# Performance work log

Measured on AMD Instinct MI355X. Metric: run time of the kernel, lower is better.

## Reference

```python
import jax, jax.numpy as jnp
import numpy as np

CLASS_INTERVAL = 4.0
CLASS_RANGE = 24.0
EPS = 1e-8


def rotate_half(x):
    # pairs adjacent elements: (x0,x1)->(-x1,x0)
    x = x.reshape(x.shape[:-1] + (x.shape[-1] // 2, 2))
    x1, x2 = x[..., 0], x[..., 1]
    return jnp.stack((-x2, x1), axis=-1).reshape(x.shape[:-2] + (-1,))


def rope_1d(x, pos):
    # x: [B, H, N, hd], pos: [N]
    hd = x.shape[-1]
    freqs = 1.0 / (10000.0 ** (jnp.arange(0, hd, 2)[: hd // 2].astype(jnp.float32) / hd))
    f = pos.astype(jnp.float32)[:, None] * freqs[None, :]   # [N, hd/2]
    f = jnp.repeat(f, 2, axis=-1)                            # [N, hd] interleaved
    cos = jnp.cos(f)[None, None]
    sin = jnp.sin(f)[None, None]
    xf = x.astype(jnp.float32)
    return (xf * cos + rotate_half(xf) * sin).astype(x.dtype)


def normalize_and_scale(col, src_min, src_max, tgt_min, tgt_max):
    return (col - src_min) / (src_max - src_min + EPS) * (tgt_max - tgt_min) + tgt_min


def setup_inputs() -> dict:
    key = jax.random.key(0)
    ks = jax.random.split(key, 9)
    N_t, N_h, N_w = 21, 30, 52
    S = N_h * N_w
    dim, enc_dim, N_a = 1536, 768, 32
    scale = 0.02
    return {
        "x": jax.random.normal(ks[0], (1, N_t * S, dim), jnp.float32),
        "encoder_hidden_states": jax.random.normal(ks[1], (N_t, N_a, enc_dim), jnp.float32),
        "x_ref_attn_map": jax.random.uniform(ks[2], (2, N_t * S), jnp.float32),
        "q_w": jax.random.normal(ks[3], (dim, dim), jnp.float32) * scale,
        "q_b": jax.random.normal(ks[4], (dim,), jnp.float32) * scale,
        "kv_w": jax.random.normal(ks[5], (2 * dim, enc_dim), jnp.float32) * scale,
        "kv_b": jax.random.normal(ks[6], (2 * dim,), jnp.float32) * scale,
        "proj_w": jax.random.normal(ks[7], (dim, dim), jnp.float32) * scale,
        "proj_b": jax.random.normal(ks[8], (dim,), jnp.float32) * scale,
        "N_t": N_t,
        "N_h": N_h,
        "N_w": N_w,
        "human_num": 2,
    }


def reference(x, encoder_hidden_states, x_ref_attn_map, q_w, q_b, kv_w, kv_b,
              proj_w, proj_b, N_t, N_h, N_w, human_num):
    assert human_num == 2
    B_orig = x.shape[0]
    S = N_h * N_w
    dim = x.shape[-1]
    num_heads = 12
    head_dim = dim // num_heads
    B = B_orig * N_t

    xf = x.reshape(B, S, dim)                                  # (B*N_t, S, C)
    q = (xf @ q_w.T + q_b).reshape(B, S, num_heads, head_dim)
    q = jnp.transpose(q, (0, 2, 1, 3))                         # [B, H, S, hd]

    # ---- per-pixel speaker routing -> rotary positions (2-speaker branch) ----
    rope_h1 = (0.0, CLASS_INTERVAL)
    rope_h2 = (CLASS_RANGE - CLASS_INTERVAL, CLASS_RANGE)
    rope_bak = CLASS_RANGE / 2.0
    m = x_ref_attn_map                                          # [2, N_t*S]
    human1 = normalize_and_scale(m[0], m[0].min(), m[0].max(), *rope_h1)
    human2 = normalize_and_scale(m[1], m[1].min(), m[1].max(), *rope_h2)
    back = jnp.full_like(human1, rope_bak)
    normalized_map = jnp.stack([human1, human2, back], axis=1)  # [N, 3]
    max_indices = jnp.argmax(m, axis=0)                         # [N]
    normalized_pos = jnp.take_along_axis(normalized_map, max_indices[:, None], axis=1)[:, 0]

    # RoPE on queries over the full (N_t*S) token axis
    q = q.reshape(B_orig, N_t, num_heads, S, head_dim)
    q = jnp.transpose(q, (0, 2, 1, 3, 4)).reshape(B_orig, num_heads, N_t * S, head_dim)
    q = rope_1d(q, normalized_pos)
    q = q.reshape(B_orig, num_heads, N_t, S, head_dim)
    q = jnp.transpose(q, (0, 2, 1, 3, 4)).reshape(B, num_heads, S, head_dim)

    # ---- KV from encoder states, bucket-centre RoPE on K ----
    N_a = encoder_hidden_states.shape[1]
    kv = encoder_hidden_states @ kv_w.T + kv_b                  # [B, N_a, 2*dim]
    kv = kv.reshape(B, N_a, 2, num_heads, head_dim)
    k = jnp.transpose(kv[:, :, 0], (0, 2, 1, 3))                # [B, H, N_a, hd]
    v = jnp.transpose(kv[:, :, 1], (0, 2, 1, 3))

    per_frame = jnp.where(jnp.arange(N_a) < N_a // 2,
                          (rope_h1[0] + rope_h1[1]) / 2.0,
                          (rope_h2[0] + rope_h2[1]) / 2.0).astype(jnp.float32)
    encoder_pos = jnp.tile(per_frame, N_t)                      # [N_t*N_a]

    k = k.reshape(B_orig, N_t, num_heads, N_a, head_dim)
    k = jnp.transpose(k, (0, 2, 1, 3, 4)).reshape(B_orig, num_heads, N_t * N_a, head_dim)
    k = rope_1d(k, encoder_pos)
    k = k.reshape(B_orig, num_heads, N_t, N_a, head_dim)
    k = jnp.transpose(k, (0, 2, 1, 3, 4)).reshape(B, num_heads, N_a, head_dim)

    # ---- cross-attention (KV length is tiny; Q dominates traffic) ----
    scores = jnp.einsum('bhqd,bhkd->bhqk', q, k) / jnp.sqrt(jnp.float32(head_dim))
    probs = jax.nn.softmax(scores, axis=-1)
    out = jnp.einsum('bhqk,bhkd->bqhd', probs, v)               # [B, S, H, hd]

    out = out.reshape(B, S, dim) @ proj_w.T + proj_b
    return out.reshape(B_orig, N_t * S, dim)
```

## Files before the change

kernel.cpp:

```cpp
#include <hip/hip_runtime.h>
#include <cstdio>
#include <cstdint>

#define TOK   32760
#define DIM   1536
#define ENCD  768
#define NA    32
#define NT    21
#define SS    1560
#define HEADS 12
#define HD    128
#define KVROWS (NT * NA)

using f32x4  = __attribute__((ext_vector_type(4))) float;
using bf16x8 = __attribute__((ext_vector_type(8))) short;

__device__ __forceinline__ ushort bf16hi(float f) {
  unsigned u = __float_as_uint(f);
  return (ushort)((u + 0x7FFFu + ((u >> 16) & 1u)) >> 16);
}
__device__ __forceinline__ float bf16tof(ushort h) {
  return __uint_as_float(((unsigned)h) << 16);
}

__device__ __forceinline__ void gload16(const void* g, void* l) {
  __builtin_amdgcn_global_load_lds((const __attribute__((address_space(1))) void*)g,
                                   (__attribute__((address_space(3))) void*)l,
                                   16, 0, 0);
}

__global__ __launch_bounds__(1024) void minmax_pos_kernel(
    const float* __restrict__ m, float* __restrict__ pos, int N) {
  __shared__ float red[4][16];
  __shared__ float fin[4];
  int tid = threadIdx.x;
  float mn0 = 3.4e38f, mx0 = -3.4e38f, mn1 = 3.4e38f, mx1 = -3.4e38f;
  for (int i = tid; i < N; i += 1024) {
    float a = m[i], b = m[N + i];
    mn0 = fminf(mn0, a); mx0 = fmaxf(mx0, a);
    mn1 = fminf(mn1, b); mx1 = fmaxf(mx1, b);
  }
  #pragma unroll
  for (int o = 32; o >= 1; o >>= 1) {
    mn0 = fminf(mn0, __shfl_xor(mn0, o)); mx0 = fmaxf(mx0, __shfl_xor(mx0, o));
    mn1 = fminf(mn1, __shfl_xor(mn1, o)); mx1 = fmaxf(mx1, __shfl_xor(mx1, o));
  }
  int wid = tid >> 6, ln = tid & 63;
  if (ln == 0) { red[0][wid] = mn0; red[1][wid] = mx0; red[2][wid] = mn1; red[3][wid] = mx1; }
  __syncthreads();
  if (tid == 0) {
    float a = red[0][0], b = red[1][0], c = red[2][0], d = red[3][0];
    for (int i = 1; i < 16; i++) {
      a = fminf(a, red[0][i]); b = fmaxf(b, red[1][i]);
      c = fminf(c, red[2][i]); d = fmaxf(d, red[3][i]);
    }
    fin[0] = a; fin[1] = b; fin[2] = c; fin[3] = d;
  }
  __syncthreads();
  float mn0f = fin[0], sc0 = 4.0f / (fin[1] - fin[0] + 1e-8f);
  float mn1f = fin[2], sc1 = 4.0f / (fin[3] - fin[2] + 1e-8f);
  for (int i = tid; i < N; i += 1024) {
    float a = m[i], b = m[N + i];
    float h1 = (a - mn0f) * sc0;
    float h2 = (b - mn1f) * sc1 + 20.0f;
    pos[i] = (a >= b) ? h1 : h2;
  }
}

__global__ void conv_hilo_kernel(const float* __restrict__ in, ushort* __restrict__ out,
                                 int M, int K) {
  int total4 = M * (K / 4);
  for (int idx = blockIdx.x * blockDim.x + threadIdx.x; idx < total4;
       idx += gridDim.x * blockDim.x) {
    int e = idx * 4;
    int row = e / K;
    int k = e - row * K;
    float4 v = *(const float4*)(in + e);
    float fs[4] = {v.x, v.y, v.z, v.w};
    ushort hs[4], ls[4];
    #pragma unroll
    for (int t = 0; t < 4; t++) {
      hs[t] = bf16hi(fs[t]);
      float hf = bf16tof(hs[t]);
      ls[t] = bf16hi(fs[t] - hf);
    }
    ushort* po = out + (size_t)row * (2 * K) + k;
    *(ushort4*)(po)     = make_ushort4(hs[0], hs[1], hs[2], hs[3]);
    *(ushort4*)(po + K) = make_ushort4(ls[0], ls[1], ls[2], ls[3]);
  }
}

__global__ __launch_bounds__(256, 2) void gemm_bf16s_kernel(
    const ushort* __restrict__ A, const ushort* __restrict__ B,
    const float* __restrict__ bias, float* __restrict__ C,
    int M, int N, int K) {
  __shared__ __align__(16) ushort lAh[128][64];
  __shared__ __align__(16) ushort lAl[128][64];
  __shared__ __align__(16) ushort lBh[128][64];
  __shared__ __align__(16) ushort lBl[128][64];
  const int tid = threadIdx.x;
  const int lane = tid & 63;
  const int w = tid >> 6;
  const int wm = w >> 1, wn = w & 1;
  const int quad = lane >> 4, m16 = lane & 15;
  const int r_off = lane >> 3;
  const int g     = lane & 7;
  const int gg8   = (g ^ r_off) * 8;

  int bx = blockIdx.x, by = blockIdx.y;
  {
    const int nx = gridDim.x, ny = gridDim.y;
    if ((ny & 7) == 0) {
      int flat = by * nx + bx;
      int xcd = flat & 7, s = flat >> 3;
      int panel = s / nx;
      bx = s - panel * nx;
      by = panel * 8 + xcd;
    }
  }
  const int m0 = by * 128, n0 = bx * 128;
  const int lda = 2 * K;

  f32x4 acc[4][4];
  #pragma unroll
  for (int i = 0; i < 4; i++)
    #pragma unroll
    for (int j = 0; j < 4; j++) acc[i][j] = (f32x4){0.f, 0.f, 0.f, 0.f};

  const int nIter = K / 64;
  for (int kt = 0; kt < nIter; kt++) {
    const int kH = kt * 64;
    const int kL = K + kt * 64;
    __syncthreads();
    #pragma unroll
    for (int i = 0; i < 4; i++) {
      const int ss = w * 4 + i;
      int rowA = m0 + ss * 8 + r_off; if (rowA >= M) rowA = M - 1;
      const ushort* ar = A + (size_t)rowA * lda;
      gload16(ar + kH + gg8, (char*)&lAh[0][0] + ss * 1024);
      gload16(ar + kL + gg8, (char*)&lAl[0][0] + ss * 1024);
      int rowB = n0 + ss * 8 + r_off; if (rowB >= N) rowB = N - 1;
      const ushort* br = B + (size_t)rowB * lda;
      gload16(br + kH + gg8, (char*)&lBh[0][0] + ss * 1024);
      gload16(br + kL + gg8, (char*)&lBl[0][0] + ss * 1024);
    }
    __syncthreads();
    #pragma unroll
    for (int kk = 0; kk < 2; kk++) {
      const int slot8 = (((kk * 4 + quad) ^ (m16 & 7)) * 8);
      bf16x8 fah[4], fbh[4], ft[4];
      #pragma unroll
      for (int i = 0; i < 4; i++) {
        fah[i] = *(const bf16x8*)(&lAh[wm * 64 + i * 16 + m16][slot8]);
        fbh[i] = *(const bf16x8*)(&lBh[wn * 64 + i * 16 + m16][slot8]);
      }
      #pragma unroll
      for (int i = 0; i < 4; i++)
        #pragma unroll
        for (int j = 0; j < 4; j++)
          acc[i][j] = __builtin_amdgcn_mfma_f32_16x16x32_bf16(fah[i], fbh[j], acc[i][j], 0, 0, 0);
      #pragma unroll
      for (int i = 0; i < 4; i++)
        ft[i] = *(const bf16x8*)(&lBl[wn * 64 + i * 16 + m16][slot8]);
      #pragma unroll
      for (int i = 0; i < 4; i++)
        #pragma unroll
        for (int j = 0; j < 4; j++)
          acc[i][j] = __builtin_amdgcn_mfma_f32_16x16x32_bf16(fah[i], ft[j], acc[i][j], 0, 0, 0);
      #pragma unroll
      for (int i = 0; i < 4; i++)
        ft[i] = *(const bf16x8*)(&lAl[wm * 64 + i * 16 + m16][slot8]);
      #pragma unroll
      for (int i = 0; i < 4; i++)
        #pragma unroll
        for (int j = 0; j < 4; j++)
          acc[i][j] = __builtin_amdgcn_mfma_f32_16x16x32_bf16(ft[i], fbh[j], acc[i][j], 0, 0, 0);
    }
  }
  #pragma unroll
  for (int j = 0; j < 4; j++) {
    const int col = n0 + wn * 64 + j * 16 + m16;
    const float bv = bias[col];
    #pragma unroll
    for (int i = 0; i < 4; i++) {
      const int rbase = m0 + wm * 64 + i * 16 + quad * 4;
      #pragma unroll
      for (int r = 0; r < 4; r++) {
        const int row = rbase + r;
        if (row < M) C[(size_t)row * N + col] = acc[i][j][r] + bv;
      }
    }
  }
}

__global__ __launch_bounds__(512, 2) void gemm256_bf16s_kernel(
    const ushort* __restrict__ A, const ushort* __restrict__ B,
    const float* __restrict__ bias, float* __restrict__ C,
    int M, int N, int K) {
  __shared__ __align__(16) ushort SA[2][256][64];
  __shared__ __align__(16) ushort SB[2][256][64];
  const int tid  = threadIdx.x;
  const int lane = tid & 63;
  const int w    = tid >> 6;
  const int wm   = w >> 2, wn = w & 3;
  const int quad = lane >> 4, m16 = lane & 15;
  const int rsel = lane >> 3;
  const int q    = (lane & 7) ^ rsel;
  int bx = blockIdx.x, by = blockIdx.y;
  {
    const int nx = gridDim.x, ny = gridDim.y;
    if ((ny & 7) == 0) {
      int flat = by * nx + bx;
      int xcd = flat & 7, s = flat >> 3;
      int panel = s / nx;
      bx = s - panel * nx;
      by = panel * 8 + xcd;
    }
  }
  const int m0 = by * 256, n0 = bx * 256;
  const int ld   = 2 * K;
  const int qoff = (q & 3) * 8 + (q >> 2) * K;
  const int shq  = (quad ^ (m16 & 7)) * 8;

  auto stageA = [&](int st, int r0) {
    int R = m0 + r0 + rsel; if (R >= M) R = M - 1;
    gload16(A + (size_t)R * ld + qoff + st * 32, &SA[st & 1][r0][0]);
  };
  auto stageB = [&](int st, int r0) {
    int R = n0 + r0 + rsel; if (R >= N) R = N - 1;
    gload16(B + (size_t)R * ld + qoff + st * 32, &SB[st & 1][r0][0]);
  };
  auto c1 = [&](int st) {
    int G = 2 * w;
    stageB(st, 32 + (G >> 2) * 64 + (G & 3) * 8); G++;
    stageB(st, 32 + (G >> 2) * 64 + (G & 3) * 8);
  };
  auto c2 = [&](int st) {
    int G = 2 * w;
    stageA(st, (G & 7) * 8 + (G >> 3) * 128); G++;
    stageA(st, (G & 7) * 8 + (G >> 3) * 128);
  };
  auto c3 = [&](int st) {
    int G = 2 * w;
    stageA(st, 64 + (G & 7) * 8 + (G >> 3) * 128); G++;
    stageA(st, 64 + (G & 7) * 8 + (G >> 3) * 128);
  };
  auto c4 = [&](int st) {
    int G = 2 * w;
    stageB(st, (G >> 2) * 64 + (G & 3) * 8); G++;
    stageB(st, (G >> 2) * 64 + (G & 3) * 8);
  };

  f32x4 acc[8][4];
  #pragma unroll
  for (int i = 0; i < 8; i++)
    #pragma unroll
    for (int j = 0; j < 4; j++) acc[i][j] = (f32x4){0.f, 0.f, 0.f, 0.f};

  const int nS = K / 32;
  c1(0); c2(0); c3(0); c4(0);
  c1(1); c2(1);
  asm volatile("s_waitcnt vmcnt(4)" ::: "memory");
  __builtin_amdgcn_s_barrier();
  asm volatile("" ::: "memory");

#define PHASE(MH, NH, PF)                                                     \
  {                                                                           \
    PF;                                                                       \
    bf16x8 ah[4], al[4], bh[2], bl[2];                                        \
    _Pragma("unroll")                                                         \
    for (int i = 0; i < 4; i++) {                                             \
      const ushort* ar = &SA[bb][wm * 128 + (MH) * 64 + i * 16 + m16][0];     \
      ah[i] = *(const bf16x8*)(ar + shq);                                     \
      al[i] = *(const bf16x8*)(ar + (shq ^ 32));                              \
    }                                                                         \
    _Pragma("unroll")                                                         \
    for (int j = 0; j < 2; j++) {                                             \
      const ushort* br = &SB[bb][wn * 64 + (NH) * 32 + j * 16 + m16][0];      \
      bh[j] = *(const bf16x8*)(br + shq);                                     \
      bl[j] = *(const bf16x8*)(br + (shq ^ 32));                              \
    }                                                                         \
    __builtin_amdgcn_s_barrier();                                             \
    asm volatile("" ::: "memory");                                            \
    __builtin_amdgcn_s_setprio(1);                                            \
    _Pragma("unroll")                                                         \
    for (int i = 0; i < 4; i++)                                               \
      _Pragma("unroll")                                                       \
      for (int j = 0; j < 2; j++)                                             \
        acc[(MH) * 4 + i][(NH) * 2 + j] = __builtin_amdgcn_mfma_f32_16x16x32_bf16( \
            ah[i], bh[j], acc[(MH) * 4 + i][(NH) * 2 + j], 0, 0, 0);          \
    _Pragma("unroll")                                                         \
    for (int i = 0; i < 4; i++)                                               \
      _Pragma("unroll")                                                       \
      for (int j = 0; j < 2; j++)                                             \
        acc[(MH) * 4 + i][(NH) * 2 + j] = __builtin_amdgcn_mfma_f32_16x16x32_bf16( \
            ah[i], bl[j], acc[(MH) * 4 + i][(NH) * 2 + j], 0, 0, 0);          \
    _Pragma("unroll")                                                         \
    for (int i = 0; i < 4; i++)                                               \
      _Pragma("unroll")                                                       \
      for (int j = 0; j < 2; j++)                                             \
        acc[(MH) * 4 + i][(NH) * 2 + j] = __builtin_amdgcn_mfma_f32_16x16x32_bf16( \
            al[i], bh[j], acc[(MH) * 4 + i][(NH) * 2 + j], 0, 0, 0);          \
    __builtin_amdgcn_s_setprio(0);                                            \
  }

  for (int s = 0; s < nS; s++) {
    const int bb = s & 1;
    PHASE(0, 1, if (s + 1 < nS) c3(s + 1));
    asm volatile("s_waitcnt lgkmcnt(0)" ::: "memory");
    __builtin_amdgcn_s_barrier();
    asm volatile("" ::: "memory");
    PHASE(1, 1, if (s + 1 < nS) c4(s + 1));
    asm volatile("s_waitcnt lgkmcnt(0)" ::: "memory");
    __builtin_amdgcn_s_barrier();
    asm volatile("" ::: "memory");
    PHASE(0, 0, if (s + 2 < nS) c1(s + 2));
    asm volatile("s_waitcnt lgkmcnt(0)" ::: "memory");
    __builtin_amdgcn_s_barrier();
    asm volatile("" ::: "memory");
    PHASE(1, 0, if (s + 2 < nS) c2(s + 2));
    asm volatile("s_waitcnt lgkmcnt(0)" ::: "memory");
    if (s + 2 < nS) { asm volatile("s_waitcnt vmcnt(4)" ::: "memory"); }
    else            { asm volatile("s_waitcnt vmcnt(0)" ::: "memory"); }
    __builtin_amdgcn_s_barrier();
    asm volatile("" ::: "memory");
  }
#undef PHASE

  #pragma unroll
  for (int J = 0; J < 4; J++) {
    const int col = n0 + wn * 64 + J * 16 + m16;
    const float bv = bias[col];
    #pragma unroll
    for (int I = 0; I < 8; I++) {
      const int rbase = m0 + wm * 128 + I * 16 + quad * 4;
      #pragma unroll
      for (int r = 0; r < 4; r++) {
        const int row = rbase + r;
        if (row < M) C[(size_t)row * N + col] = acc[I][J][r] + bv;
      }
    }
  }
}

__global__ __launch_bounds__(64) void attn_kernel(
    const float* __restrict__ q, const float* __restrict__ kv,
    const float* __restrict__ pos, ushort* __restrict__ attA) {
  const int chunk = blockIdx.x;
  const int head  = blockIdx.y;
  const int t     = blockIdx.z;
  const int lane  = threadIdx.x;
  const int a = lane & 31, h = lane >> 5;
  const float L2_10000_64 = 13.287712379549449f / 64.0f;

  float kreg[64];
  const float* krow = kv + (size_t)(t * NA + a) * (2 * DIM) + head * HD + h * 64;
  #pragma unroll
  for (int j = 0; j < 16; j++) ((float4*)kreg)[j] = ((const float4*)krow)[j];
  const float pk = (a < 16) ? 2.0f : 22.0f;
  #pragma unroll
  for (int j = 0; j < 32; j++) {
    int ip = h * 32 + j;
    float fr = exp2f(-(float)ip * L2_10000_64);
    float sn, cs; sincosf(pk * fr, &sn, &cs);
    float x0 = kreg[2 * j], x1 = kreg[2 * j + 1];
    kreg[2 * j]     = x0 * cs - x1 * sn;
    kreg[2 * j + 1] = x1 * cs + x0 * sn;
  }
  float vr0[32], vr1[32];
  const float* vbase = kv + (size_t)(t * NA) * (2 * DIM) + DIM + head * HD;
  #pragma unroll
  for (int aa = 0; aa < 32; aa++) {
    vr0[aa] = vbase[(size_t)aa * (2 * DIM) + lane];
    vr1[aa] = vbase[(size_t)aa * (2 * DIM) + 64 + lane];
  }

  __shared__ float qs[128];
  __shared__ float Ps[32];
  const float myfreq = exp2f(-(float)lane * L2_10000_64);

  for (int r = 0; r < 30; r++) {
    const int n = t * SS + chunk * 30 + r;
    float2 qp = ((const float2*)(q + (size_t)n * DIM + head * HD))[lane];
    float p = pos[n];
    float sn, cs; sincosf(p * myfreq, &sn, &cs);
    qs[2 * lane]     = qp.x * cs - qp.y * sn;
    qs[2 * lane + 1] = qp.y * cs + qp.x * sn;
    __syncthreads();
    float accd = 0.f;
    #pragma unroll
    for (int j4 = 0; j4 < 16; j4++) {
      float4 qq = ((const float4*)(qs + h * 64))[j4];
      accd += qq.x * kreg[j4 * 4] + qq.y * kreg[j4 * 4 + 1] +
              qq.z * kreg[j4 * 4 + 2] + qq.w * kreg[j4 * 4 + 3];
    }
    accd += __shfl_xor(accd, 32);
    accd *= 0.08838834764831845f;
    float mx = accd;
    #pragma unroll
    for (int o = 16; o >= 1; o >>= 1) mx = fmaxf(mx, __shfl_xor(mx, o));
    float e = __expf(accd - mx);
    float sum = e;
    #pragma unroll
    for (int o = 16; o >= 1; o >>= 1) sum += __shfl_xor(sum, o);
    float P = e / sum;
    if (lane < 32) Ps[lane] = P;
    __syncthreads();
    float o0 = 0.f, o1 = 0.f;
    #pragma unroll
    for (int aa = 0; aa < 32; aa++) {
      float pa = Ps[aa];
      o0 += pa * vr0[aa];
      o1 += pa * vr1[aa];
    }
    size_t base = (size_t)n * (2 * DIM);
    int c0 = head * HD + lane;
    ushort h0 = bf16hi(o0); ushort l0 = bf16hi(o0 - bf16tof(h0));
    ushort h1 = bf16hi(o1); ushort l1 = bf16hi(o1 - bf16tof(h1));
    attA[base + c0]            = h0;
    attA[base + DIM + c0]      = l0;
    attA[base + c0 + 64]       = h1;
    attA[base + DIM + c0 + 64] = l1;
    __syncthreads();
  }
}

extern "C" void kernel_launch(void* const* d_in, const int* in_sizes, int n_in,
                              void* d_out, int out_size, void* d_ws, size_t ws_size,
                              hipStream_t stream) {
  const float* x      = (const float*)d_in[0];
  const float* enc    = (const float*)d_in[1];
  const float* xmap   = (const float*)d_in[2];
  const float* q_w    = (const float*)d_in[3];
  const float* q_b    = (const float*)d_in[4];
  const float* kv_w   = (const float*)d_in[5];
  const float* kv_b   = (const float*)d_in[6];
  const float* proj_w = (const float*)d_in[7];
  const float* proj_b = (const float*)d_in[8];
  float* out = (float*)d_out;
  char* ws = (char*)d_ws;

  const size_t OFF_POS  = 0;
  const size_t OFF_APR  = 131072;
  const size_t OFF_Q    = OFF_APR + 201277440;
  const size_t OFF_KV   = OFF_Q   + 201277440;
  const size_t OFF_BQ   = OFF_KV  + 8257536;
  const size_t OFF_BKV  = OFF_BQ  + 9437184;
  const size_t OFF_BP   = OFF_BKV + 9437184;
  const size_t OFF_AKV  = OFF_BP  + 9437184;
  const size_t TOTAL    = OFF_AKV + 2064384;
  if (ws_size < TOTAL) {
    fprintf(stderr, "kernel_launch: ws_size %zu < needed %zu\n", ws_size, TOTAL);
    return;
  }
  float*  pos   = (float*)(ws + OFF_POS);
  ushort* Apr   = (ushort*)(ws + OFF_APR);
  float*  qbuf  = (float*)(ws + OFF_Q);
  float*  kvbuf = (float*)(ws + OFF_KV);
  ushort* Bq    = (ushort*)(ws + OFF_BQ);
  ushort* Bkv   = (ushort*)(ws + OFF_BKV);
  ushort* Bp    = (ushort*)(ws + OFF_BP);
  ushort* Akv   = (ushort*)(ws + OFF_AKV);

  minmax_pos_kernel<<<1, 1024, 0, stream>>>(xmap, pos, TOK);
  conv_hilo_kernel<<<2048, 256, 0, stream>>>(x,      Apr, TOK,    DIM);
  conv_hilo_kernel<<<256,  256, 0, stream>>>(q_w,    Bq,  DIM,    DIM);
  conv_hilo_kernel<<<256,  256, 0, stream>>>(kv_w,   Bkv, 2*DIM,  ENCD);
  conv_hilo_kernel<<<64,   256, 0, stream>>>(enc,    Akv, KVROWS, ENCD);
  conv_hilo_kernel<<<256,  256, 0, stream>>>(proj_w, Bp,  DIM,    DIM);
  gemm256_bf16s_kernel<<<dim3(DIM/256, (TOK+255)/256), 512, 0, stream>>>(
      Apr, Bq, q_b, qbuf, TOK, DIM, DIM);
  gemm_bf16s_kernel<<<dim3(2*DIM/128, (KVROWS+127)/128), 256, 0, stream>>>(
      Akv, Bkv, kv_b, kvbuf, KVROWS, 2*DIM, ENCD);
  attn_kernel<<<dim3(52, HEADS, NT), 64, 0, stream>>>(qbuf, kvbuf, pos, Apr);
  gemm256_bf16s_kernel<<<dim3(DIM/256, (TOK+255)/256), 512, 0, stream>>>(
      Apr, Bp, proj_b, out, TOK, DIM, DIM);
}
```

Baseline: 1.917 ms.

## Replace four-phase interleaved GEMM pipeline with single-phase double-buffered loop

Replaces the 4-phase per-K-step schedule, which interleaved partial global prefetches with quarter-tile MFMA blocks and barriers, with one phase per step. Each step loads all A/B fragments from LDS, runs the full 8x4 MFMA block, then issues the whole prefetch for step s+2 behind a single barrier. This cuts barriers per K-step from four to one or two and simplifies the waitcnt logic. In exchange it loses the fine-grained overlap of global loads with compute and raises fragment register pressure (8+8+4+4 bf16x8 live at once), which could lower occupancy or cause spills.

Result: faster. 1.699 ms (-11.3%).

```diff
diff --git a/kernel.cpp b/kernel.cpp
--- a/kernel.cpp
+++ b/kernel.cpp
@@ -230,26 +230,13 @@
     int R = n0 + r0 + rsel; if (R >= N) R = N - 1;
     gload16(B + (size_t)R * ld + qoff + st * 32, &SB[st & 1][r0][0]);
   };
-  auto c1 = [&](int st) {
-    int G = 2 * w;
-    stageB(st, 32 + (G >> 2) * 64 + (G & 3) * 8); G++;
-    stageB(st, 32 + (G >> 2) * 64 + (G & 3) * 8);
+  auto stage = [&](int st) {
+    #pragma unroll
+    for (int t = 0; t < 4; t++) {
+      stageA(st, w * 32 + t * 8);
+      stageB(st, w * 32 + t * 8);
+    }
   };
-  auto c2 = [&](int st) {
-    int G = 2 * w;
-    stageA(st, (G & 7) * 8 + (G >> 3) * 128); G++;
-    stageA(st, (G & 7) * 8 + (G >> 3) * 128);
-  };
-  auto c3 = [&](int st) {
-    int G = 2 * w;
-    stageA(st, 64 + (G & 7) * 8 + (G >> 3) * 128); G++;
-    stageA(st, 64 + (G & 7) * 8 + (G >> 3) * 128);
-  };
-  auto c4 = [&](int st) {
-    int G = 2 * w;
-    stageB(st, (G >> 2) * 64 + (G & 3) * 8); G++;
-    stageB(st, (G >> 2) * 64 + (G & 3) * 8);
-  };
 
   f32x4 acc[8][4];
   #pragma unroll
@@ -258,74 +245,62 @@
     for (int j = 0; j < 4; j++) acc[i][j] = (f32x4){0.f, 0.f, 0.f, 0.f};
 
   const int nS = K / 32;
-  c1(0); c2(0); c3(0); c4(0);
-  c1(1); c2(1);
-  asm volatile("s_waitcnt vmcnt(4)" ::: "memory");
+  stage(0);
+  if (nS > 1) {
+    stage(1);
+    asm volatile("s_waitcnt vmcnt(8)" ::: "memory");
+  } else {
+    asm volatile("s_waitcnt vmcnt(0)" ::: "memory");
+  }
   __builtin_amdgcn_s_barrier();
   asm volatile("" ::: "memory");
 
-#define PHASE(MH, NH, PF)                                                     \
-  {                                                                           \
-    PF;                                                                       \
-    bf16x8 ah[4], al[4], bh[2], bl[2];                                        \
-    _Pragma("unroll")                                                         \
-    for (int i = 0; i < 4; i++) {                                             \
-      const ushort* ar = &SA[bb][wm * 128 + (MH) * 64 + i * 16 + m16][0];     \
-      ah[i] = *(const bf16x8*)(ar + shq);                                     \
-      al[i] = *(const bf16x8*)(ar + (shq ^ 32));                              \
-    }                                                                         \
-    _Pragma("unroll")                                                         \
-    for (int j = 0; j < 2; j++) {                                             \
-      const ushort* br = &SB[bb][wn * 64 + (NH) * 32 + j * 16 + m16][0];      \
-      bh[j] = *(const bf16x8*)(br + shq);                                     \
-      bl[j] = *(const bf16x8*)(br + (shq ^ 32));                              \
-    }                                                                         \
-    __builtin_amdgcn_s_barrier();                                             \
-    asm volatile("" ::: "memory");                                            \
-    __builtin_amdgcn_s_setprio(1);                                            \
-    _Pragma("unroll")                                                         \
-    for (int i = 0; i < 4; i++)                                               \
-      _Pragma("unroll")                                                       \
-      for (int j = 0; j < 2; j++)                                             \
-        acc[(MH) * 4 + i][(NH) * 2 + j] = __builtin_amdgcn_mfma_f32_16x16x32_bf16( \
-            ah[i], bh[j], acc[(MH) * 4 + i][(NH) * 2 + j], 0, 0, 0);          \
-    _Pragma("unroll")                                                         \
-    for (int i = 0; i < 4; i++)                                               \
-      _Pragma("unroll")                                                       \
-      for (int j = 0; j < 2; j++)                                             \
-        acc[(MH) * 4 + i][(NH) * 2 + j] = __builtin_amdgcn_mfma_f32_16x16x32_bf16( \
-            ah[i], bl[j], acc[(MH) * 4 + i][(NH) * 2 + j], 0, 0, 0);          \
-    _Pragma("unroll")                                                         \
-    for (int i = 0; i < 4; i++)                                               \
-      _Pragma("unroll")                                                       \
-      for (int j = 0; j < 2; j++)                                             \
-        acc[(MH) * 4 + i][(NH) * 2 + j] = __builtin_amdgcn_mfma_f32_16x16x32_bf16( \
-            al[i], bh[j], acc[(MH) * 4 + i][(NH) * 2 + j], 0, 0, 0);          \
-    __builtin_amdgcn_s_setprio(0);                                            \
-  }
-
   for (int s = 0; s < nS; s++) {
     const int bb = s & 1;
-    PHASE(0, 1, if (s + 1 < nS) c3(s + 1));
+    bf16x8 ah[8], al[8], bh[4], bl[4];
+    #pragma unroll
+    for (int i = 0; i < 8; i++) {
+      const ushort* ar = &SA[bb][wm * 128 + i * 16 + m16][0];
+      ah[i] = *(const bf16x8*)(ar + shq);
+      al[i] = *(const bf16x8*)(ar + (shq ^ 32));
+    }
+    #pragma unroll
+    for (int j = 0; j < 4; j++) {
+      const ushort* br = &SB[bb][wn * 64 + j * 16 + m16][0];
+      bh[j] = *(const bf16x8*)(br + shq);
+      bl[j] = *(const bf16x8*)(br + (shq ^ 32));
+    }
+    __builtin_amdgcn_s_setprio(1);
+    #pragma unroll
+    for (int i = 0; i < 8; i++)
+      #pragma unroll
+      for (int j = 0; j < 4; j++)
+        acc[i][j] = __builtin_amdgcn_mfma_f32_16x16x32_bf16(ah[i], bh[j], acc[i][j], 0, 0, 0);
+    #pragma unroll
+    for (int i = 0; i < 8; i++)
+      #pragma unroll
+      for (int j = 0; j < 4; j++)
+        acc[i][j] = __builtin_amdgcn_mfma_f32_16x16x32_bf16(ah[i], bl[j], acc[i][j], 0, 0, 0);
+    #pragma unroll
+    for (int i = 0; i < 8; i++)
+      #pragma unroll
+      for (int j = 0; j < 4; j++)
+        acc[i][j] = __builtin_amdgcn_mfma_f32_16x16x32_bf16(al[i], bh[j], acc[i][j], 0, 0, 0);
+    __builtin_amdgcn_s_setprio(0);
     asm volatile("s_waitcnt lgkmcnt(0)" ::: "memory");
     __builtin_amdgcn_s_barrier();
     asm volatile("" ::: "memory");
-    PHASE(1, 1, if (s + 1 < nS) c4(s + 1));
-    asm volatile("s_waitcnt lgkmcnt(0)" ::: "memory");
-    __builtin_amdgcn_s_barrier();
-    asm volatile("" ::: "memory");
-    PHASE(0, 0, if (s + 2 < nS) c1(s + 2));
-    asm volatile("s_waitcnt lgkmcnt(0)" ::: "memory");
-    __builtin_amdgcn_s_barrier();
-    asm volatile("" ::: "memory");
-    PHASE(1, 0, if (s + 2 < nS) c2(s + 2));
-    asm volatile("s_waitcnt lgkmcnt(0)" ::: "memory");
-    if (s + 2 < nS) { asm volatile("s_waitcnt vmcnt(4)" ::: "memory"); }
-    else            { asm volatile("s_waitcnt vmcnt(0)" ::: "memory"); }
-    __builtin_amdgcn_s_barrier();
-    asm volatile("" ::: "memory");
-  }
-#undef PHASE
+    if (s + 2 < nS) {
+      stage(s + 2);
+      asm volatile("s_waitcnt vmcnt(8)" ::: "memory");
+      __builtin_amdgcn_s_barrier();
+      asm volatile("" ::: "memory");
+    } else if (s + 1 < nS) {
+      asm volatile("s_waitcnt vmcnt(0)" ::: "memory");
+      __builtin_amdgcn_s_barrier();
+      asm volatile("" ::: "memory");
+    }
+  }
 
   #pragma unroll
   for (int J = 0; J < 4; J++) {
```
